# Kernel optimization log

Measured on AMD Instinct MI355X. Metric: run time of the kernel, lower is better.

The kernel has to match this reference:

```python
import jax, jax.numpy as jnp
import numpy as np

N, E, B, M = 50000, 100000, 50, 50
NPG = N // B            # atoms per graph
DIN, H1, H2, DE, AAF, G = 32, 32, 64, 16, 95, 128
K, T = 3, 6             # ARMA num_stacks, num_layers
F1, F2, F3 = 64, 32, 16
EA = 2 * (M - 1)        # amino-acid edges per graph


def setup_inputs() -> dict:
    key = jax.random.key(0)
    ks = jax.random.split(key, 24)
    s = 0.05
    def w(k, shape):
        return jax.random.normal(k, shape, jnp.float32) * s
    return {
        "x": jax.random.normal(ks[0], (N, DIN), jnp.float32),
        "edge_attr": jax.random.normal(ks[1], (E, DE), jnp.float32),
        "aa_features": jax.random.normal(ks[2], (B, M, AAF), jnp.float32),
        "edge_index": jax.random.randint(ks[3], (2, E), 0, N),
        "monomer_labels": jax.random.randint(ks[4], (B, NPG), 0, M),
        "amino_edge_index": jax.random.randint(ks[5], (2, EA), 0, M),
        "W_e1": w(ks[6], (DE, DIN * H1)), "b_e1": jnp.zeros((DIN * H1,), jnp.float32),
        "root1": w(ks[7], (DIN, H1)), "bias1": jnp.zeros((H1,), jnp.float32),
        "W_e2": w(ks[8], (DE, H1 * H2)), "b_e2": jnp.zeros((H1 * H2,), jnp.float32),
        "root2": w(ks[9], (H1, H2)), "bias2": jnp.zeros((H2,), jnp.float32),
        "Wa_atom": w(ks[10], (H2, 1)), "ba_atom": jnp.zeros((1,), jnp.float32),
        "arma_init_w": w(ks[11], (K, H2 + AAF, G)),
        "arma_w": w(ks[12], (T - 1, K, G, G)),
        "arma_root_w": w(ks[13], (T, K, H2 + AAF, G)),
        "arma_bias": jnp.zeros((T, K, G), jnp.float32),
        "Wa_aa": w(ks[14], (G, 1)), "ba_aa": jnp.zeros((1,), jnp.float32),
        "W1": w(ks[15], (G, F1)), "b1": jnp.zeros((F1,), jnp.float32),
        "W2": w(ks[16], (F1, F2)), "b2": jnp.zeros((F2,), jnp.float32),
        "W3": w(ks[17], (F2, F3)), "b3": jnp.zeros((F3,), jnp.float32),
        "W4": w(ks[18], (F3, 1)), "b4": jnp.zeros((1,), jnp.float32),
    }


def _nnconv(h, src, dst, edge_attr, Wm, bm, root, bias, fin, fout):
    # NNConv (aggr='add'): edge MLP -> per-edge weight matrix, gather-matmul-scatter
    w_e = (edge_attr @ Wm + bm).reshape(-1, fin, fout)            # [E, fin, fout]
    msg = jnp.einsum('ef,efo->eo', h[src], w_e)                   # [E, fout]
    agg = jax.ops.segment_sum(msg, dst, num_segments=h.shape[0])  # scatter-add to targets
    return agg + h @ root + bias


def _forward(x, edge_attr, aa_features, W_e1, b_e1, root1, bias1, W_e2, b_e2, root2, bias2,
             Wa_atom, ba_atom, arma_init_w, arma_w, arma_root_w, arma_bias, Wa_aa, ba_aa,
             W1, b1, W2, b2, W3, b3, W4, b4, edge_index, monomer_labels, amino_edge_index):
    src, dst = edge_index[0], edge_index[1]
    h = jax.nn.relu(_nnconv(x, src, dst, edge_attr, W_e1, b_e1, root1, bias1, DIN, H1))
    h = jax.nn.relu(_nnconv(h, src, dst, edge_attr, W_e2, b_e2, root2, bias2, H1, H2))

    # per-graph attention readout over atoms -> amino-acid embeddings (scatter by monomer label)
    xg = h.reshape(B, NPG, H2)
    attn = jax.nn.softmax(xg @ Wa_atom + ba_atom, axis=1)         # softmax over atoms in graph
    wx = xg * attn
    aa = jax.vmap(lambda wxi, lbl: jax.ops.segment_sum(wxi, lbl, num_segments=M))(wx, monomer_labels)
    h_aa = jnp.concatenate([aa, aa_features], axis=-1)            # [B, M, H2+95]

    # ARMAConv: gcn_norm without self-loops on amino-acid graph (shared across graphs)
    asrc, adst = amino_edge_index[0], amino_edge_index[1]
    deg = jax.ops.segment_sum(jnp.ones((EA,), x.dtype), adst, num_segments=M)
    dinv = jnp.where(deg > 0, 1.0 / jnp.sqrt(jnp.maximum(deg, 1.0)), 0.0)
    norm = dinv[asrc] * dinv[adst]                                # [EA]

    def arma(x0):  # x0: [M, H2+95]
        out = jnp.einsum('mf,kfo->kmo', x0, arma_init_w)          # [K, M, G]
        for t in range(T):
            if t > 0:
                out = jnp.einsum('kmo,kop->kmp', out, arma_w[t - 1])
            msg = out[:, asrc] * norm[None, :, None]              # [K, EA, G]
            prop = jax.vmap(lambda m: jax.ops.segment_sum(m, adst, num_segments=M))(msg)
            rootc = jnp.einsum('mf,kfo->kmo', x0, arma_root_w[t])
            out = jax.nn.relu(prop + rootc + arma_bias[t][:, None, :])
        return out.mean(axis=0)                                   # mean over stacks -> [M, G]

    g = jax.vmap(arma)(h_aa)                                      # [B, M, G]

    # attention readout over amino acids
    attn2 = jax.nn.softmax(g @ Wa_aa + ba_aa, axis=1)
    p = jnp.sum(g * attn2, axis=1)                                # [B, G]

    p = jax.nn.relu(p @ W1 + b1)
    p = jax.nn.relu(p @ W2 + b2)
    p = jax.nn.relu(p @ W3 + b3)
    p = p @ W4 + b4
    return p.reshape(-1)                                          # [B]


def reference(x, edge_attr, aa_features, edge_index, monomer_labels, amino_edge_index,
              W_e1, b_e1, root1, bias1, W_e2, b_e2, root2, bias2, Wa_atom, ba_atom,
              arma_init_w, arma_w, arma_root_w, arma_bias, Wa_aa, ba_aa,
              W1, b1, W2, b2, W3, b3, W4, b4):
    return _forward(x, edge_attr, aa_features, W_e1, b_e1, root1, bias1, W_e2, b_e2, root2, bias2,
                    Wa_atom, ba_atom, arma_init_w, arma_w, arma_root_w, arma_bias, Wa_aa, ba_aa,
                    W1, b1, W2, b2, W3, b3, W4, b4, edge_index, monomer_labels, amino_edge_index)
```

## Files before the change

### kernel.cpp

```cpp
#include <hip/hip_runtime.h>
#include <math.h>

#define N_ATOMS 50000
#define E_EDGES 100000
#define B_G     50
#define M_M     50
#define NPG     1000
#define DIN     32
#define H1C     32
#define H2C     64
#define DEC     16
#define AAF     95
#define G_DIM   128
#define K_ST    3
#define T_L     6
#define EA_E    98
#define XDIM    159
#define NS      21
#define MPAD    64
#define GP      132
#define GPS     136
#define KP2     168
#define KW      544
#define SLC     10
#define APB     100
#define NSB     ((N_ATOMS + 255) / 256)

#define OFF_WE2 (H1C * KW)
#define OFF_WT  (OFF_WE2 + H2C * KW)
#define OFF_AW  (OFF_WT + NS * XDIM * G_DIM)
#define OFF_DEG (OFF_AW + (T_L - 1) * K_ST * G_DIM * G_DIM)
#define PREP_TOTAL (OFF_DEG + E_EDGES)

typedef __attribute__((ext_vector_type(8))) short bf16x8;
typedef __attribute__((ext_vector_type(4))) float f32x4;
typedef __attribute__((ext_vector_type(4))) unsigned int u32x4;

__device__ __forceinline__ short f2bf(float f) {
    unsigned int u = __float_as_uint(f);
    unsigned int r = (u + 0x7FFFu + ((u >> 16) & 1u)) >> 16;
    return (short)r;
}
__device__ __forceinline__ float bf2f(short b) {
    return __uint_as_float(((unsigned int)(unsigned short)b) << 16);
}
__device__ __forceinline__ unsigned int cvtpk_bf16(float lo, float hi) {
    unsigned int r;
    asm("v_cvt_pk_bf16_f32 %0, %1, %2" : "=v"(r) : "v"(lo), "v"(hi));
    return r;
}

__device__ __forceinline__ void f4fma(float4& d, float s, const float4& v) {
    d.x += s * v.x; d.y += s * v.y; d.z += s * v.z; d.w += s * v.w;
}
__device__ __forceinline__ void f4add(float4& d, const float4& v) {
    d.x += v.x; d.y += v.y; d.z += v.z; d.w += v.w;
}
__device__ __forceinline__ void f4relu(float4& d) {
    d.x = fmaxf(d.x, 0.f); d.y = fmaxf(d.y, 0.f);
    d.z = fmaxf(d.z, 0.f); d.w = fmaxf(d.w, 0.f);
}

__global__ __launch_bounds__(256) void prep_all(
    const float* __restrict__ We1, const float* __restrict__ be1, short* __restrict__ WB1,
    const float* __restrict__ We2, const float* __restrict__ be2, short* __restrict__ WB2,
    const float* __restrict__ init_w, const float* __restrict__ root_w, short* __restrict__ Wtb,
    const float* __restrict__ arma_w, short* __restrict__ Wab,
    const int* __restrict__ eidx, int* __restrict__ deg,
    const int* __restrict__ aei, int* __restrict__ aa_off,
    int* __restrict__ aa_src, float* __restrict__ aa_nrm)
{
    int tid = threadIdx.x;
    if (blockIdx.x == 0) {
        __shared__ int   sdeg[M_M];
        __shared__ int   scur[M_M];
        __shared__ float sdinv[M_M];
        __shared__ int   soff[M_M + 1];
        if (tid < M_M) { sdeg[tid] = 0; scur[tid] = 0; }
        __syncthreads();
        if (tid < EA_E) atomicAdd(&sdeg[aei[EA_E + tid]], 1);
        __syncthreads();
        if (tid < M_M) {
            float dv = (float)sdeg[tid];
            sdinv[tid] = (dv > 0.f) ? (1.f / sqrtf(fmaxf(dv, 1.f))) : 0.f;
        }
        __syncthreads();
        if (tid == 0) {
            soff[0] = 0;
            for (int m = 0; m < M_M; ++m) soff[m + 1] = soff[m] + sdeg[m];
        }
        __syncthreads();
        if (tid < EA_E) {
            int ss = aei[tid], dd = aei[EA_E + tid];
            int pos = atomicAdd(&scur[dd], 1);
            int idx = soff[dd] + pos;
            aa_src[idx] = ss;
            aa_nrm[idx] = sdinv[ss] * sdinv[dd];
        }
        if (tid < M_M + 1) aa_off[tid] = soff[tid];
        return;
    }
    int idx = (blockIdx.x - 1) * 256 + tid;
    if (idx < OFF_WE2) {
        int o = idx / KW, k = idx - o * KW;
        float v = (k < 512) ? We1[(size_t)k * H1C + o]
                            : be1[(size_t)(k - 512) * H1C + o];
        WB1[idx] = f2bf(v);
    } else if (idx < OFF_WT) {
        int rem = idx - OFF_WE2;
        int o = rem / KW, k = rem - o * KW;
        float v = (k < 512) ? We2[(size_t)k * H2C + o]
                            : be2[(size_t)(k - 512) * H2C + o];
        WB2[rem] = f2bf(v);
    } else if (idx < OFF_AW) {
        int rem = idx - OFF_WT;
        int s = rem / (XDIM * G_DIM);
        int r2 = rem - s * XDIM * G_DIM;
        int k = r2 / G_DIM, n = r2 - k * G_DIM;
        float v = (s < K_ST) ? init_w[rem]
                             : root_w[(size_t)(s - K_ST) * XDIM * G_DIM + r2];
        Wtb[(size_t)s * G_DIM * KP2 + n * KP2 + k] = f2bf(v);
    } else if (idx < OFF_DEG) {
        int rem = idx - OFF_AW;
        int slot = rem / (G_DIM * G_DIM);
        int r2 = rem - slot * G_DIM * G_DIM;
        int p = r2 / G_DIM, n = r2 - p * G_DIM;
        Wab[(size_t)slot * G_DIM * G_DIM + n * G_DIM + p] = f2bf(arma_w[rem]);
    } else if (idx < PREP_TOTAL) {
        int e = idx - OFF_DEG;
        atomicAdd(&deg[eidx[E_EDGES + e]], 1);
    }
}

__global__ __launch_bounds__(256) void scan_part(const int* __restrict__ deg,
                                                 int* __restrict__ bsum)
{
    __shared__ int tmp[256];
    int tid = threadIdx.x;
    int n = blockIdx.x * 256 + tid;
    tmp[tid] = (n < N_ATOMS) ? deg[n] : 0;
    __syncthreads();
    for (int off = 128; off > 0; off >>= 1) {
        if (tid < off) tmp[tid] += tmp[tid + off];
        __syncthreads();
    }
    if (tid == 0) bsum[blockIdx.x] = tmp[0];
}

__global__ __launch_bounds__(256) void scan_mid(const int* __restrict__ bsum,
                                                int* __restrict__ bpre)
{
    __shared__ int tmp[256];
    int tid = threadIdx.x;
    int v = (tid < NSB) ? bsum[tid] : 0;
    tmp[tid] = v;
    __syncthreads();
    for (int off = 1; off < 256; off <<= 1) {
        int t = tmp[tid];
        int add = (tid >= off) ? tmp[tid - off] : 0;
        __syncthreads();
        tmp[tid] = t + add;
        __syncthreads();
    }
    if (tid < NSB) bpre[tid] = tmp[tid] - v;
}

__global__ __launch_bounds__(256) void scan_out(int* __restrict__ deg_off,
                                                const int* __restrict__ bpre)
{
    __shared__ int tmp[256];
    int tid = threadIdx.x;
    int n = blockIdx.x * 256 + tid;
    int v = (n < N_ATOMS) ? deg_off[n] : 0;
    tmp[tid] = v;
    __syncthreads();
    for (int off = 1; off < 256; off <<= 1) {
        int t = tmp[tid];
        int add = (tid >= off) ? tmp[tid - off] : 0;
        __syncthreads();
        tmp[tid] = t + add;
        __syncthreads();
    }
    int incl = tmp[tid];
    int base = bpre[blockIdx.x];
    if (n < N_ATOMS) deg_off[n] = base + incl - v;
    if (n == N_ATOMS - 1) deg_off[N_ATOMS] = base + incl;
}

template<int FOUT, int NTT, int WGRP, int MTB, bool CIPOS>
__global__ __launch_bounds__(256) void edge_msg_v2(
    const float* __restrict__ h, const float* __restrict__ ea,
    const int* __restrict__ eidx, int* __restrict__ ipos,
    const int* __restrict__ off, int* __restrict__ cursor,
    const short* __restrict__ WB, float* __restrict__ msg)
{
    constexpr int KS = 17;
    __shared__ int iplds[MTB * 16];
    int tid  = threadIdx.x;
    int lane = tid & 63, wave = tid >> 6;
    int l16  = lane & 15, quad = lane >> 4;
    int nt   = wave % NTT, tg = wave / NTT;
    int ebase = blockIdx.x * (MTB * 16);

    if (CIPOS) {
        if (tid < MTB * 16) {
            int e = ebase + tid;
            if (e < E_EDGES) {
                int d = eidx[E_EDGES + e];
                int pos = atomicAdd(&cursor[d], 1);
                int p = off[d] + pos;
                iplds[tid] = p;
                ipos[e] = p;
            }
        }
    }

    bf16x8 Bfr[KS];
    {
        const short* wb = WB + (size_t)(nt * 16 + l16) * KW;
        #pragma unroll
        for (int ks = 0; ks < KS; ++ks)
            Bfr[ks] = *(const bf16x8*)(wb + ks * 32 + quad * 8);
    }
    if (CIPOS) __syncthreads();

    for (int t = tg; t < MTB; t += WGRP) {
        int e  = ebase + t * 16 + l16;
        int es = (e < E_EDGES) ? e : (E_EDGES - 1);
        int s  = eidx[es];
        float4 h0 = *(const float4*)(h + (size_t)s * 32 + quad * 8);
        float4 h1 = *(const float4*)(h + (size_t)s * 32 + quad * 8 + 4);
        float hf[8] = {h0.x, h0.y, h0.z, h0.w, h1.x, h1.y, h1.z, h1.w};
        float4 e0 = *(const float4*)(ea + (size_t)es * DEC);
        float4 e1 = *(const float4*)(ea + (size_t)es * DEC + 4);
        float4 e2 = *(const float4*)(ea + (size_t)es * DEC + 8);
        float4 e3 = *(const float4*)(ea + (size_t)es * DEC + 12);
        float eaf[16] = {e0.x, e0.y, e0.z, e0.w, e1.x, e1.y, e1.z, e1.w,
                         e2.x, e2.y, e2.z, e2.w, e3.x, e3.y, e3.z, e3.w};

        f32x4 acc = (f32x4){0.f, 0.f, 0.f, 0.f};
        #pragma unroll
        for (int ks = 0; ks < KS; ++ks) {
            u32x4 av;
            if (ks < DEC) {
                float fac = eaf[ks];
                #pragma unroll
                for (int j = 0; j < 4; ++j)
                    av[j] = cvtpk_bf16(fac * hf[2 * j], fac * hf[2 * j + 1]);
            } else {
                #pragma unroll
                for (int j = 0; j < 4; ++j)
                    av[j] = cvtpk_bf16(hf[2 * j], hf[2 * j + 1]);
            }
            bf16x8 a = __builtin_bit_cast(bf16x8, av);
            acc = __builtin_amdgcn_mfma_f32_16x16x32_bf16(a, Bfr[ks], acc, 0, 0, 0);
        }
        int erb = ebase + t * 16 + quad * 4;
        #pragma unroll
        for (int r = 0; r < 4; ++r) {
            int ee = erb + r;
            if (ee < E_EDGES) {
                int p = CIPOS ? iplds[t * 16 + quad * 4 + r] : ipos[ee];
                msg[(size_t)p * FOUT + nt * 16 + l16] = acc[r];
            }
        }
    }
}

template<int FIN, int FOUT, bool SCORE>
__global__ __launch_bounds__(256) void gather_update(
    const float* __restrict__ msg, const int* __restrict__ off,
    const float* __restrict__ hin,
    const float* __restrict__ root, const float* __restrict__ bias,
    float* __restrict__ hout,
    const float* __restrict__ wa, const float* __restrict__ ba,
    float* __restrict__ sc)
{
    constexpr int NPB = 256 / FOUT;
    __shared__ float rlds[FIN][FOUT];
    __shared__ float hlds[NPB][FIN];
    int tid = threadIdx.x;
    for (int i = tid; i < FIN * FOUT / 4; i += 256) {
        *(float4*)&rlds[0][i * 4] = *(const float4*)(root + i * 4);
    }
    int nb = blockIdx.x * NPB;
    for (int i = tid; i < NPB * FIN; i += 256) {
        int ln = i / FIN, f = i % FIN;
        int n = nb + ln;
        hlds[ln][f] = (n < N_ATOMS) ? hin[(size_t)n * FIN + f] : 0.f;
    }
    __syncthreads();

    int ln = tid / FOUT, o = tid % FOUT;
    int n = nb + ln;
    if (n >= N_ATOMS) return;
    float acc = bias[o];
    #pragma unroll 8
    for (int f = 0; f < FIN; ++f) acc += hlds[ln][f] * rlds[f][o];
    int j0 = off[n], j1 = off[n + 1];
    for (int j = j0; j < j1; ++j) {
        acc += msg[(size_t)j * FOUT + o];
    }
    float hv = fmaxf(acc, 0.f);
    hout[(size_t)n * FOUT + o] = hv;
    if constexpr (SCORE) {
        static_assert(FOUT == 64, "score fusion needs node==wave");
        float sv = hv * wa[o];
        #pragma unroll
        for (int d = 32; d > 0; d >>= 1) sv += __shfl_down(sv, d);
        if (o == 0) sc[n] = sv + ba[0];
    }
}

__global__ __launch_bounds__(256) void atom_scatter_sm(
    const float* __restrict__ h2, const float* __restrict__ sc,
    const int* __restrict__ labels, float* __restrict__ partial)
{
    __shared__ float aa4[4][M_M][H2C];
    __shared__ float red[256];
    int b = blockIdx.x / SLC, s = blockIdx.x % SLC;
    int tid = threadIdx.x;
    int wave = tid >> 6, lane = tid & 63;
    const float* sb = sc + (size_t)b * NPG;

    for (int i = tid; i < 4 * M_M * H2C; i += 256) ((float*)aa4)[i] = 0.f;

    float lmax = -1e30f;
    for (int n = tid; n < NPG; n += 256) lmax = fmaxf(lmax, sb[n]);
    red[tid] = lmax;
    __syncthreads();
    for (int off = 128; off > 0; off >>= 1) {
        if (tid < off) red[tid] = fmaxf(red[tid], red[tid + off]);
        __syncthreads();
    }
    float mx = red[0];
    __syncthreads();
    float lsum = 0.f;
    for (int n = tid; n < NPG; n += 256) lsum += expf(sb[n] - mx);
    red[tid] = lsum;
    __syncthreads();
    for (int off = 128; off > 0; off >>= 1) {
        if (tid < off) red[tid] += red[tid + off];
        __syncthreads();
    }
    float inv = 1.f / red[0];
    __syncthreads();

    int nbase = s * APB;
    const float* hb = h2 + (size_t)b * NPG * H2C;
    #pragma unroll 5
    for (int it = 0; it < APB / 4; ++it) {
        int n = nbase + it * 4 + wave;
        int lbl = labels[b * NPG + n];
        float w = expf(sb[n] - mx) * inv;
        float hv = hb[(size_t)n * H2C + lane];
        aa4[wave][lbl][lane] += hv * w;
    }
    __syncthreads();
    float* pb = partial + (size_t)(b * SLC + s) * M_M * H2C;
    for (int i = tid; i < M_M * H2C; i += 256) {
        float v = ((float*)aa4)[i] + ((float*)aa4)[M_M * H2C + i]
                + ((float*)aa4)[2 * M_M * H2C + i] + ((float*)aa4)[3 * M_M * H2C + i];
        pb[i] = v;
    }
}

__global__ __launch_bounds__(256) void x0_finalize(
    const float* __restrict__ partial, const float* __restrict__ aaf,
    short* __restrict__ x0b)
{
    int idx = blockIdx.x * 256 + threadIdx.x;
    if (idx >= B_G * MPAD * KP2) return;
    int b = idx / (MPAD * KP2);
    int rem = idx - b * (MPAD * KP2);
    int m = rem / KP2, k = rem - m * KP2;
    float v = 0.f;
    if (m < M_M) {
        if (k < H2C) {
            const float* pb = partial + (size_t)b * SLC * M_M * H2C + m * H2C + k;
            #pragma unroll
            for (int s = 0; s < SLC; ++s) v += pb[(size_t)s * (M_M * H2C)];
        } else if (k < XDIM) {
            v = aaf[((size_t)b * M_M + m) * AAF + (k - H2C)];
        }
    }
    x0b[idx] = f2bf(v);
}

__global__ __launch_bounds__(256, 1) void arma_iter(
    const short* __restrict__ x0b, const short* __restrict__ Wtb,
    const short* __restrict__ Wab, const float* __restrict__ arma_bias,
    const int* __restrict__ aa_off, const int* __restrict__ aa_src,
    const float* __restrict__ aa_nrm, float* __restrict__ gfull)
{
    __shared__ float Abuf[MPAD][GP];
    __shared__ float Rall[3][MPAD][GP];
    __shared__ short Bb16[MPAD][GPS];
    __shared__ int   s_off[M_M + 1];
    __shared__ int   s_src[EA_E];
    __shared__ float s_nrm[EA_E];
    int b = blockIdx.x / K_ST, k = blockIdx.x % K_ST;
    int tid = threadIdx.x;
    int oi = tid & 15, mi = tid >> 4;
    int c0 = oi * 4, c1 = 64 + oi * 4;
    int lane = tid & 63, wave = tid >> 6;
    int l16 = lane & 15, quad = lane >> 4;
    int w2 = wave >> 1, nh = wave & 1;

    if (tid < M_M + 1) s_off[tid] = aa_off[tid];
    if (tid < EA_E) { s_src[tid] = aa_src[tid]; s_nrm[tid] = aa_nrm[tid]; }
    for (int i = tid; i < MPAD * GPS / 2; i += 256) {
        ((int*)Bb16)[i] = 0;
    }

    bf16x8 Afr[2][5];
    #pragma unroll
    for (int h = 0; h < 2; ++h) {
        int mt = w2 + 2 * h;
        const short* xb = x0b + (size_t)b * MPAD * KP2 + (mt * 16 + l16) * KP2;
        #pragma unroll
        for (int ks = 0; ks < 5; ++ks)
            Afr[h][ks] = *(const bf16x8*)(xb + ks * 32 + quad * 8);
    }

    auto x0_gemm = [&](const short* __restrict__ W, float (*dst)[GP]) {
        bf16x8 Bfr[5][4];
        #pragma unroll
        for (int ks = 0; ks < 5; ++ks)
            #pragma unroll
            for (int nt = 0; nt < 4; ++nt)
                Bfr[ks][nt] = *(const bf16x8*)(W +
                    (size_t)((nh * 4 + nt) * 16 + l16) * KP2 + ks * 32 + quad * 8);
        #pragma unroll
        for (int h = 0; h < 2; ++h) {
            int mt = w2 + 2 * h;
            f32x4 acc[4];
            #pragma unroll
            for (int nt = 0; nt < 4; ++nt) acc[nt] = (f32x4){0.f, 0.f, 0.f, 0.f};
            #pragma unroll
            for (int ks = 0; ks < 5; ++ks)
                #pragma unroll
                for (int nt = 0; nt < 4; ++nt)
                    acc[nt] = __builtin_amdgcn_mfma_f32_16x16x32_bf16(
                        Afr[h][ks], Bfr[ks][nt], acc[nt], 0, 0, 0);
            #pragma unroll
            for (int nt = 0; nt < 4; ++nt)
                #pragma unroll
                for (int r = 0; r < 4; ++r)
                    dst[mt * 16 + quad * 4 + r][(nh * 4 + nt) * 16 + l16] = acc[nt][r];
        }
    };

    x0_gemm(Wtb + (size_t)k * G_DIM * KP2, Abuf);
    #pragma unroll
    for (int t = 0; t < 3; ++t)
        x0_gemm(Wtb + (size_t)(K_ST + t * K_ST + k) * G_DIM * KP2, Rall[t]);

    float* gb = gfull + ((size_t)(b * K_ST + k)) * M_M * G_DIM;
    __syncthreads();

    #pragma unroll
    for (int t = 0; t < T_L; ++t) {
        if (t > 0) {
            const short* aw = Wab + (size_t)((t - 1) * K_ST + k) * G_DIM * G_DIM;
            bf16x8 Wfr[4][4];
            #pragma unroll
            for (int ks = 0; ks < 4; ++ks)
                #pragma unroll
                for (int nt = 0; nt < 4; ++nt)
                    Wfr[ks][nt] = *(const bf16x8*)(aw +
                        (size_t)((nh * 4 + nt) * 16 + l16) * G_DIM + ks * 32 + quad * 8);
            #pragma unroll
            for (int h = 0; h < 2; ++h) {
                int mt = w2 + 2 * h;
                f32x4 acc[4];
                #pragma unroll
                for (int nt = 0; nt < 4; ++nt) acc[nt] = (f32x4){0.f, 0.f, 0.f, 0.f};
                #pragma unroll
                for (int ks = 0; ks < 4; ++ks) {
                    bf16x8 a = *(const bf16x8*)&Bb16[mt * 16 + l16][ks * 32 + quad * 8];
                    #pragma unroll
                    for (int nt = 0; nt < 4; ++nt)
                        acc[nt] = __builtin_amdgcn_mfma_f32_16x16x32_bf16(
                            a, Wfr[ks][nt], acc[nt], 0, 0, 0);
                }
                #pragma unroll
                for (int nt = 0; nt < 4; ++nt)
                    #pragma unroll
                    for (int r = 0; r < 4; ++r)
                        Abuf[mt * 16 + quad * 4 + r][(nh * 4 + nt) * 16 + l16] = acc[nt][r];
            }
            if (t == 3) {
                #pragma unroll
                for (int tt = 3; tt < 6; ++tt)
                    x0_gemm(Wtb + (size_t)(K_ST + tt * K_ST + k) * G_DIM * KP2,
                            Rall[tt - 3]);
            }
            __syncthreads();
        }
        const float (*Rb)[GP] = Rall[t % 3];
        const float* bb = arma_bias + ((size_t)t * K_ST + k) * G_DIM;
        float4 bias0 = *(const float4*)(bb + c0);
        float4 bias1 = *(const float4*)(bb + c1);
        #pragma unroll
        for (int r = 0; r < 4; ++r) {
            int m = mi * 4 + r;
            if (m < M_M) {
                float4 v0 = bias0, v1 = bias1;
                f4add(v0, *(const float4*)&Rb[m][c0]);
                f4add(v1, *(const float4*)&Rb[m][c1]);
                int j0 = s_off[m], j1 = s_off[m + 1];
                for (int j = j0; j < j1; ++j) {
                    float nv = s_nrm[j];
                    const float* ap = &Abuf[s_src[j]][0];
                    f4fma(v0, nv, *(const float4*)(ap + c0));
                    f4fma(v1, nv, *(const float4*)(ap + c1));
                }
                f4relu(v0);
                f4relu(v1);
                unsigned int p0 = cvtpk_bf16(v0.x, v0.y);
                unsigned int p1 = cvtpk_bf16(v0.z, v0.w);
                unsigned int p2 = cvtpk_bf16(v1.x, v1.y);
                unsigned int p3 = cvtpk_bf16(v1.z, v1.w);
                *(uint2*)&Bb16[m][c0] = make_uint2(p0, p1);
                *(uint2*)&Bb16[m][c1] = make_uint2(p2, p3);
                if (t == T_L - 1) {
                    *(float4*)(gb + m * G_DIM + c0) = v0;
                    *(float4*)(gb + m * G_DIM + c1) = v1;
                }
            }
        }
        __syncthreads();
    }
}

__global__ __launch_bounds__(128) void aa_readout_mlp(
    const float* __restrict__ gfull, const float* __restrict__ wa,
    const float* __restrict__ ba,
    const float* __restrict__ W1, const float* __restrict__ b1,
    const float* __restrict__ W2, const float* __restrict__ b2,
    const float* __restrict__ W3, const float* __restrict__ b3,
    const float* __restrict__ W4, const float* __restrict__ b4,
    float* __restrict__ out)
{
    __shared__ float g[M_M][G_DIM + 1];
    __shared__ float s2[M_M];
    __shared__ float p[G_DIM];
    __shared__ float r1[64], r2[32], r3[16];
    int b = blockIdx.x, tid = threadIdx.x;
    const float* g0 = gfull + (size_t)b * K_ST * M_M * G_DIM;
    for (int i = tid; i < M_M * G_DIM; i += 128) {
        int m = i >> 7, o = i & 127;
        g[m][o] = (g0[i] + g0[M_M*G_DIM + i] + g0[2*M_M*G_DIM + i]) * (1.f/3.f);
    }
    __syncthreads();
    if (tid < M_M) {
        float sv = ba[0];
        for (int o = 0; o < G_DIM; ++o) sv += g[tid][o] * wa[o];
        s2[tid] = sv;
    }
    __syncthreads();
    if (tid == 0) {
        float mx = -1e30f;
        for (int m = 0; m < M_M; ++m) mx = fmaxf(mx, s2[m]);
        float den = 0.f;
        for (int m = 0; m < M_M; ++m) den += expf(s2[m] - mx);
        float inv = 1.f / den;
        for (int m = 0; m < M_M; ++m) s2[m] = expf(s2[m] - mx) * inv;
    }
    __syncthreads();
    {
        float pv = 0.f;
        for (int m = 0; m < M_M; ++m) pv += g[m][tid] * s2[m];
        p[tid] = pv;
    }
    __syncthreads();
    if (tid < 64) {
        float v = b1[tid];
        for (int i = 0; i < 128; ++i) v += p[i] * W1[i * 64 + tid];
        r1[tid] = fmaxf(v, 0.f);
    }
    __syncthreads();
    if (tid < 32) {
        float v = b2[tid];
        for (int i = 0; i < 64; ++i) v += r1[i] * W2[i * 32 + tid];
        r2[tid] = fmaxf(v, 0.f);
    }
    __syncthreads();
    if (tid < 16) {
        float v = b3[tid];
        for (int i = 0; i < 32; ++i) v += r2[i] * W3[i * 16 + tid];
        r3[tid] = fmaxf(v, 0.f);
    }
    __syncthreads();
    if (tid == 0) {
        float v = b4[0];
        for (int i = 0; i < 16; ++i) v += r3[i] * W4[i];
        out[b] = v;
    }
}

extern "C" void kernel_launch(void* const* d_in, const int* in_sizes, int n_in,
                              void* d_out, int out_size, void* d_ws, size_t ws_size,
                              hipStream_t stream)
{
    (void)in_sizes; (void)n_in; (void)out_size; (void)ws_size;
    const float* x            = (const float*)d_in[0];
    const float* edge_attr    = (const float*)d_in[1];
    const float* aa_features  = (const float*)d_in[2];
    const int*   edge_index   = (const int*)  d_in[3];
    const int*   mono_labels  = (const int*)  d_in[4];
    const int*   amino_ei     = (const int*)  d_in[5];
    const float* W_e1 = (const float*)d_in[6];
    const float* b_e1 = (const float*)d_in[7];
    const float* root1= (const float*)d_in[8];
    const float* bias1= (const float*)d_in[9];
    const float* W_e2 = (const float*)d_in[10];
    const float* b_e2 = (const float*)d_in[11];
    const float* root2= (const float*)d_in[12];
    const float* bias2= (const float*)d_in[13];
    const float* Wa_atom = (const float*)d_in[14];
    const float* ba_atom = (const float*)d_in[15];
    const float* arma_init_w = (const float*)d_in[16];
    const float* arma_w      = (const float*)d_in[17];
    const float* arma_root_w = (const float*)d_in[18];
    const float* arma_bias   = (const float*)d_in[19];
    const float* Wa_aa = (const float*)d_in[20];
    const float* ba_aa = (const float*)d_in[21];
    const float* W1 = (const float*)d_in[22];
    const float* b1 = (const float*)d_in[23];
    const float* W2 = (const float*)d_in[24];
    const float* b2 = (const float*)d_in[25];
    const float* W3 = (const float*)d_in[26];
    const float* b3 = (const float*)d_in[27];
    const float* W4 = (const float*)d_in[28];
    const float* b4 = (const float*)d_in[29];

    float* ws = (float*)d_ws;
    float* h1    = ws;
    float* h2    = h1   + (size_t)N_ATOMS * H1C;
    float* h_aa  = h2   + (size_t)N_ATOMS * H2C;
    float* sc    = h_aa + (size_t)B_G * M_M * XDIM;
    int*   aa_off = (int*)(sc + (size_t)B_G * NPG);
    int*   aa_src = aa_off + (M_M + 1);
    float* aa_nrm = (float*)(aa_src + EA_E);
    int*   deg_off = (int*)(aa_nrm + EA_E);
    int*   cursor  = deg_off + (N_ATOMS + 1);
    int*   ipos    = cursor + N_ATOMS;
    int*   bsum    = ipos + E_EDGES;
    int*   bpre    = bsum + 256;
    float* RC    = (float*)(bpre + 256);
    float* gfull = RC + (size_t)B_G * NS * M_M * G_DIM;
    short* Wtb   = (short*)((((uintptr_t)(gfull + (size_t)B_G * K_ST * M_M * G_DIM)) + 15)
                            & ~(uintptr_t)15);
    short* x0b   = Wtb + (size_t)NS * G_DIM * KP2;
    short* Wab   = x0b + (size_t)B_G * MPAD * KP2;
    short* WB1   = Wab + (size_t)(T_L - 1) * K_ST * G_DIM * G_DIM;
    short* WB2   = WB1 + (size_t)H1C * KW;
    float* msg   = RC;
    float* partial = RC;
    (void)h_aa;

    (void)hipMemsetAsync(deg_off, 0, (2 * N_ATOMS + 1) * sizeof(int), stream);

    prep_all<<<1 + (PREP_TOTAL + 255) / 256, 256, 0, stream>>>(
        W_e1, b_e1, WB1, W_e2, b_e2, WB2,
        arma_init_w, arma_root_w, Wtb, arma_w, Wab,
        edge_index, deg_off, amino_ei, aa_off, aa_src, aa_nrm);

    scan_part<<<NSB, 256, 0, stream>>>(deg_off, bsum);
    scan_mid<<<1, 256, 0, stream>>>(bsum, bpre);
    scan_out<<<NSB, 256, 0, stream>>>(deg_off, bpre);

    edge_msg_v2<H1C, 2, 2, 8, true><<<(E_EDGES + 127) / 128, 256, 0, stream>>>(
        x, edge_attr, edge_index, ipos, deg_off, cursor, WB1, msg);
    gather_update<DIN, H1C, false><<<(N_ATOMS + 7) / 8, 256, 0, stream>>>(
        msg, deg_off, x, root1, bias1, h1, nullptr, nullptr, nullptr);
    edge_msg_v2<H2C, 4, 1, 8, false><<<(E_EDGES + 127) / 128, 256, 0, stream>>>(
        h1, edge_attr, edge_index, ipos, nullptr, nullptr, WB2, msg);
    gather_update<H1C, H2C, true><<<(N_ATOMS + 3) / 4, 256, 0, stream>>>(
        msg, deg_off, h1, root2, bias2, h2, Wa_atom, ba_atom, sc);

    atom_scatter_sm<<<B_G * SLC, 256, 0, stream>>>(h2, sc, mono_labels, partial);
    x0_finalize<<<(B_G * MPAD * KP2 + 255) / 256, 256, 0, stream>>>(
        partial, aa_features, x0b);

    arma_iter<<<B_G * K_ST, 256, 0, stream>>>(x0b, Wtb, Wab, arma_bias,
                                              aa_off, aa_src, aa_nrm, gfull);
    aa_readout_mlp<<<B_G, 128, 0, stream>>>(gfull, Wa_aa, ba_aa, W1, b1, W2, b2, W3, b3, W4, b4,
                                            (float*)d_out);
}
```

Measured before the change: 295.5 us.

## Replace three-pass scan with atomic-base offsets and fuse x0 finalize into scatter

The three-kernel prefix scan for the CSR offsets becomes one kernel. Each block scans locally and takes its base from a global atomic counter, so segments are contiguous but not in node order, and gather now reads aoff plus deg instead of off[n+1]. The x0_finalize kernel is folded into atom_scatter_sm with a last-block-per-graph counter and threadfences, removing another launch. The intent is fewer kernel launches and less global traffic between them, at the cost of atomic-ordering reliance and a serialized tail in the last block per graph.

```diff
diff --git a/kernel.cpp b/kernel.cpp
--- a/kernel.cpp
+++ b/kernel.cpp
@@ -132,27 +132,15 @@
     }
 }
 
-__global__ __launch_bounds__(256) void scan_part(const int* __restrict__ deg,
-                                                 int* __restrict__ bsum)
+__global__ __launch_bounds__(256) void csr_offsets(const int* __restrict__ deg,
+                                                   int* __restrict__ ecnt,
+                                                   int* __restrict__ aoff)
 {
     __shared__ int tmp[256];
+    __shared__ int base_s;
     int tid = threadIdx.x;
     int n = blockIdx.x * 256 + tid;
-    tmp[tid] = (n < N_ATOMS) ? deg[n] : 0;
-    __syncthreads();
-    for (int off = 128; off > 0; off >>= 1) {
-        if (tid < off) tmp[tid] += tmp[tid + off];
-        __syncthreads();
-    }
-    if (tid == 0) bsum[blockIdx.x] = tmp[0];
-}
-
-__global__ __launch_bounds__(256) void scan_mid(const int* __restrict__ bsum,
-                                                int* __restrict__ bpre)
-{
-    __shared__ int tmp[256];
-    int tid = threadIdx.x;
-    int v = (tid < NSB) ? bsum[tid] : 0;
+    int v = (n < N_ATOMS) ? deg[n] : 0;
     tmp[tid] = v;
     __syncthreads();
     for (int off = 1; off < 256; off <<= 1) {
@@ -162,29 +150,9 @@
         tmp[tid] = t + add;
         __syncthreads();
     }
-    if (tid < NSB) bpre[tid] = tmp[tid] - v;
-}
-
-__global__ __launch_bounds__(256) void scan_out(int* __restrict__ deg_off,
-                                                const int* __restrict__ bpre)
-{
-    __shared__ int tmp[256];
-    int tid = threadIdx.x;
-    int n = blockIdx.x * 256 + tid;
-    int v = (n < N_ATOMS) ? deg_off[n] : 0;
-    tmp[tid] = v;
-    __syncthreads();
-    for (int off = 1; off < 256; off <<= 1) {
-        int t = tmp[tid];
-        int add = (tid >= off) ? tmp[tid - off] : 0;
-        __syncthreads();
-        tmp[tid] = t + add;
-        __syncthreads();
-    }
-    int incl = tmp[tid];
-    int base = bpre[blockIdx.x];
-    if (n < N_ATOMS) deg_off[n] = base + incl - v;
-    if (n == N_ATOMS - 1) deg_off[N_ATOMS] = base + incl;
+    if (tid == 255) base_s = atomicAdd(ecnt, tmp[255]);
+    __syncthreads();
+    if (n < N_ATOMS) aoff[n] = base_s + tmp[tid] - v;
 }
 
 template<int FOUT, int NTT, int WGRP, int MTB, bool CIPOS>
@@ -269,8 +237,8 @@
 
 template<int FIN, int FOUT, bool SCORE>
 __global__ __launch_bounds__(256) void gather_update(
-    const float* __restrict__ msg, const int* __restrict__ off,
-    const float* __restrict__ hin,
+    const float* __restrict__ msg, const int* __restrict__ aoff,
+    const int* __restrict__ deg, const float* __restrict__ hin,
     const float* __restrict__ root, const float* __restrict__ bias,
     float* __restrict__ hout,
     const float* __restrict__ wa, const float* __restrict__ ba,
@@ -297,7 +265,7 @@
     float acc = bias[o];
     #pragma unroll 8
     for (int f = 0; f < FIN; ++f) acc += hlds[ln][f] * rlds[f][o];
-    int j0 = off[n], j1 = off[n + 1];
+    int j0 = aoff[n], j1 = j0 + deg[n];
     for (int j = j0; j < j1; ++j) {
         acc += msg[(size_t)j * FOUT + o];
     }
@@ -314,10 +282,13 @@
 
 __global__ __launch_bounds__(256) void atom_scatter_sm(
     const float* __restrict__ h2, const float* __restrict__ sc,
-    const int* __restrict__ labels, float* __restrict__ partial)
+    const int* __restrict__ labels, float* __restrict__ partial,
+    const float* __restrict__ aaf, short* __restrict__ x0b,
+    int* __restrict__ gcnt)
 {
     __shared__ float aa4[4][M_M][H2C];
     __shared__ float red[256];
+    __shared__ int last_s;
     int b = blockIdx.x / SLC, s = blockIdx.x % SLC;
     int tid = threadIdx.x;
     int wave = tid >> 6, lane = tid & 63;
@@ -363,28 +334,28 @@
                 + ((float*)aa4)[2 * M_M * H2C + i] + ((float*)aa4)[3 * M_M * H2C + i];
         pb[i] = v;
     }
-}
-
-__global__ __launch_bounds__(256) void x0_finalize(
-    const float* __restrict__ partial, const float* __restrict__ aaf,
-    short* __restrict__ x0b)
-{
-    int idx = blockIdx.x * 256 + threadIdx.x;
-    if (idx >= B_G * MPAD * KP2) return;
-    int b = idx / (MPAD * KP2);
-    int rem = idx - b * (MPAD * KP2);
-    int m = rem / KP2, k = rem - m * KP2;
-    float v = 0.f;
-    if (m < M_M) {
-        if (k < H2C) {
-            const float* pb = partial + (size_t)b * SLC * M_M * H2C + m * H2C + k;
-            #pragma unroll
-            for (int s = 0; s < SLC; ++s) v += pb[(size_t)s * (M_M * H2C)];
-        } else if (k < XDIM) {
-            v = aaf[((size_t)b * M_M + m) * AAF + (k - H2C)];
-        }
-    }
-    x0b[idx] = f2bf(v);
+
+    __threadfence();
+    if (tid == 0) last_s = atomicAdd(&gcnt[b], 1);
+    __syncthreads();
+    if (last_s != SLC - 1) return;
+    __threadfence();
+    const float* pbase = partial + (size_t)b * SLC * M_M * H2C;
+    short* xb = x0b + (size_t)b * MPAD * KP2;
+    for (int i = tid; i < MPAD * KP2; i += 256) {
+        int m = i / KP2, k = i - m * KP2;
+        float v = 0.f;
+        if (m < M_M) {
+            if (k < H2C) {
+                const float* pp = pbase + m * H2C + k;
+                #pragma unroll
+                for (int ss = 0; ss < SLC; ++ss) v += pp[(size_t)ss * (M_M * H2C)];
+            } else if (k < XDIM) {
+                v = aaf[((size_t)b * M_M + m) * AAF + (k - H2C)];
+            }
+        }
+        xb[i] = f2bf(v);
+    }
 }
 
 __global__ __launch_bounds__(256, 1) void arma_iter(
@@ -644,12 +615,13 @@
     int*   aa_off = (int*)(sc + (size_t)B_G * NPG);
     int*   aa_src = aa_off + (M_M + 1);
     float* aa_nrm = (float*)(aa_src + EA_E);
-    int*   deg_off = (int*)(aa_nrm + EA_E);
-    int*   cursor  = deg_off + (N_ATOMS + 1);
-    int*   ipos    = cursor + N_ATOMS;
-    int*   bsum    = ipos + E_EDGES;
-    int*   bpre    = bsum + 256;
-    float* RC    = (float*)(bpre + 256);
+    int*   deg    = (int*)(aa_nrm + EA_E);
+    int*   cursor = deg + (N_ATOMS + 1);
+    int*   ecnt   = cursor + N_ATOMS;
+    int*   gcnt   = ecnt + 1;
+    int*   ipos   = gcnt + B_G;
+    int*   aoff   = ipos + E_EDGES;
+    float* RC    = (float*)(aoff + N_ATOMS);
     float* gfull = RC + (size_t)B_G * NS * M_M * G_DIM;
     short* Wtb   = (short*)((((uintptr_t)(gfull + (size_t)B_G * K_ST * M_M * G_DIM)) + 15)
                             & ~(uintptr_t)15);
@@ -661,29 +633,26 @@
     float* partial = RC;
     (void)h_aa;
 
-    (void)hipMemsetAsync(deg_off, 0, (2 * N_ATOMS + 1) * sizeof(int), stream);
+    (void)hipMemsetAsync(deg, 0, (2 * N_ATOMS + 2 + B_G) * sizeof(int), stream);
 
     prep_all<<<1 + (PREP_TOTAL + 255) / 256, 256, 0, stream>>>(
         W_e1, b_e1, WB1, W_e2, b_e2, WB2,
         arma_init_w, arma_root_w, Wtb, arma_w, Wab,
-        edge_index, deg_off, amino_ei, aa_off, aa_src, aa_nrm);
-
-    scan_part<<<NSB, 256, 0, stream>>>(deg_off, bsum);
-    scan_mid<<<1, 256, 0, stream>>>(bsum, bpre);
-    scan_out<<<NSB, 256, 0, stream>>>(deg_off, bpre);
+        edge_index, deg, amino_ei, aa_off, aa_src, aa_nrm);
+
+    csr_offsets<<<NSB, 256, 0, stream>>>(deg, ecnt, aoff);
 
     edge_msg_v2<H1C, 2, 2, 8, true><<<(E_EDGES + 127) / 128, 256, 0, stream>>>(
-        x, edge_attr, edge_index, ipos, deg_off, cursor, WB1, msg);
+        x, edge_attr, edge_index, ipos, aoff, cursor, WB1, msg);
     gather_update<DIN, H1C, false><<<(N_ATOMS + 7) / 8, 256, 0, stream>>>(
-        msg, deg_off, x, root1, bias1, h1, nullptr, nullptr, nullptr);
+        msg, aoff, deg, x, root1, bias1, h1, nullptr, nullptr, nullptr);
     edge_msg_v2<H2C, 4, 1, 8, false><<<(E_EDGES + 127) / 128, 256, 0, stream>>>(
         h1, edge_attr, edge_index, ipos, nullptr, nullptr, WB2, msg);
     gather_update<H1C, H2C, true><<<(N_ATOMS + 3) / 4, 256, 0, stream>>>(
-        msg, deg_off, h1, root2, bias2, h2, Wa_atom, ba_atom, sc);
-
-    atom_scatter_sm<<<B_G * SLC, 256, 0, stream>>>(h2, sc, mono_labels, partial);
-    x0_finalize<<<(B_G * MPAD * KP2 + 255) / 256, 256, 0, stream>>>(
-        partial, aa_features, x0b);
+        msg, aoff, deg, h1, root2, bias2, h2, Wa_atom, ba_atom, sc);
+
+    atom_scatter_sm<<<B_G * SLC, 256, 0, stream>>>(
+        h2, sc, mono_labels, partial, aa_features, x0b, gcnt);
 
     arma_iter<<<B_G * K_ST, 256, 0, stream>>>(x0b, Wtb, Wab, arma_bias,
                                               aa_off, aa_src, aa_nrm, gfull);
```

Measured after the change: 386.5 us. 1.31x slower.
